# Performance work log

Measured on AMD Instinct MI355X. Metric: run time of the kernel, lower is better.

Reference implementation:

```python
import jax, jax.numpy as jnp
import numpy as np

L, D, NH, DH, K = 2, 128, 4, 32, 3  # blocks, latent_dim, heads, head_dim, kernel

def _ln(x, eps=1e-6):
    mu = x.mean(-1, keepdims=True)
    var = x.var(-1, keepdims=True)
    return (x - mu) / jnp.sqrt(var + eps)

def setup_inputs() -> dict:
    key = jax.random.key(0)
    ks = jax.random.split(key, 12)
    B, Hd, Wd = 2, 64, 96
    s = 0.02
    p = lambda k, shape: jax.random.normal(k, shape, jnp.float32) * s
    return {
        'feat_map': jax.random.normal(ks[0], (B, D, Hd, Wd), jnp.float32),
        'feat_map_up': jax.random.normal(ks[1], (B, D, 2 * Hd, 2 * Wd), jnp.float32),
        'nc_w': jnp.ones((L, D), jnp.float32), 'nc_b': jnp.zeros((L, D), jnp.float32),
        'wq': p(ks[2], (L, D, D)), 'bq': jnp.zeros((L, D), jnp.float32),
        'wkv': p(ks[3], (L, D, 2 * D)), 'bkv': jnp.zeros((L, 2 * D), jnp.float32),
        'wo': p(ks[4], (L, D, D)), 'bo': jnp.zeros((L, D), jnp.float32),
        'w1': p(ks[5], (L, D, 4 * D)), 'b1': jnp.zeros((L, 4 * D), jnp.float32),
        'w2': p(ks[6], (L, 4 * D, D)), 'b2': jnp.zeros((L, D), jnp.float32),
        'wqf': p(ks[7], (D, D)), 'bqf': jnp.zeros((D,), jnp.float32),
        'wcf': p(ks[8], (D, D)), 'bcf': jnp.zeros((D,), jnp.float32),
        'upsample_factor': 2,
    }

def reference(feat_map, feat_map_up, nc_w, nc_b, wq, bq, wkv, bkv, wo, bo,
              w1, b1, w2, b2, wqf, bqf, wcf, bcf, upsample_factor):
    B, C, Hd, Wd = feat_map.shape
    Hu, Wu = Hd * upsample_factor, Wd * upsample_factor
    N = B * Hu * Wu
    # ---- local 3x3 context via replicate-pad + shifted slices (== pad+unfold) ----
    pad = jnp.pad(feat_map, ((0, 0), (0, 0), (1, 1), (1, 1)), mode='edge')
    patches = jnp.stack([pad[:, :, i:i + Hd, j:j + Wd]
                         for i in range(K) for j in range(K)], axis=2)  # [B,C,9,Hd,Wd]
    # nearest-neighbor upsample by factor (== F.interpolate nearest)
    patches = jnp.repeat(jnp.repeat(patches, upsample_factor, axis=-2),
                         upsample_factor, axis=-1)                      # [B,C,9,Hu,Wu]
    context = patches.transpose(0, 3, 4, 2, 1).reshape(N, K * K, C)     # [(b h w),9,C]
    x = feat_map_up.transpose(0, 2, 3, 1).reshape(N, 1, C)              # [(b h w),1,C]
    scale = 1.0 / float(np.sqrt(DH))
    for l in range(L):
        # cross-attn: x = x + Attn(norm1(x), norm_ctx(context))
        ctx_n = _ln(context) * nc_w[l] + nc_b[l]
        q = _ln(x) @ wq[l] + bq[l]
        kv = ctx_n @ wkv[l] + bkv[l]
        k_, v_ = kv[..., :D], kv[..., D:]
        qh = q.reshape(N, 1, NH, DH).transpose(0, 2, 1, 3)       # [N,h,1,dh]
        kh = k_.reshape(N, K * K, NH, DH).transpose(0, 2, 1, 3)  # [N,h,9,dh]
        vh = v_.reshape(N, K * K, NH, DH).transpose(0, 2, 1, 3)
        attn = jax.nn.softmax(jnp.einsum('nhqd,nhkd->nhqk', qh, kh) * scale, axis=-1)
        o = jnp.einsum('nhqk,nhkd->nhqd', attn, vh).transpose(0, 2, 1, 3).reshape(N, 1, D)
        x = x + (o @ wo[l] + bo[l])
        # MLP: x = x + W2 gelu(W1 norm2(x))
        h = jax.nn.gelu(_ln(x) @ w1[l] + b1[l])  # tanh-approx gelu
        x = x + (h @ w2[l] + b2[l])
    # ---- final query-context attention mask ----
    xq = _ln(x) @ wqf + bqf
    ctxp = _ln(context) @ wcf + bcf
    logits = jnp.einsum('nqc,nkc->nqk', xq, ctxp) * (1.0 / float(np.sqrt(D)))
    attn_mask = jax.nn.softmax(logits, axis=-1)              # [N,1,9]
    return attn_mask.reshape(B, Hu, Wu, K * K).transpose(0, 3, 1, 2)  # [B,9,Hu,Wu]
```

## Files before the change

kernel.cpp:

```cpp
#include <hip/hip_runtime.h>

namespace {

constexpr int THREADS = 256;
constexpr int HdC = 64, WdC = 96, HuC = 128, WuC = 192;


__device__ __forceinline__ float gelu_tanh(float x) {
  float z = 0.7978845608028654f * (x + 0.044715f * x * x * x);
  float e = __expf(2.0f * z);
  float t = 1.0f - 2.0f / (e + 1.0f);
  return 0.5f * x * (1.0f + t);
}

__device__ __forceinline__ unsigned short f2bf(float f) {
  unsigned int u = __builtin_bit_cast(unsigned int, f);
  u = (u + 0x7FFFu + ((u >> 16) & 1u)) >> 16;
  return (unsigned short)u;
}

__device__ __forceinline__ float bf2f(unsigned short u) {
  unsigned int x = ((unsigned int)u) << 16;
  return __builtin_bit_cast(float, x);
}


constexpr int CTX_S = 80;
constexpr int KV_S  = 132;
constexpr int XS_S  = 132;
constexpr int XN_S  = 32;
constexpr int OB_S  = 144;

constexpr int SC_ATT = 0;
constexpr int SC_RED = 0;
constexpr int SC_MU  = 768;
constexpr int SC_RS  = 864;
constexpr int SC_NC  = 1152;
constexpr int SC_LG  = 0;

struct alignas(16) Smem {
  float ctxT[128 * CTX_S];
  float kvb[72 * KV_S];
  float xs[32 * XS_S];
  float xnT[128 * XN_S];
  float outb[32 * OB_S];
  float wbuf[32 * 128];
  float scratch[1536];
};
static_assert(sizeof(Smem) <= 160 * 1024, "LDS budget");

__device__ __forceinline__ void stage_w(const float* __restrict__ W, int wstride,
                                        int kc, float* wbuf, int tid) {
#pragma unroll
  for (int p = 0; p < 4; ++p) {
    int e = tid + p * THREADS;
    int r = e >> 5;
    int c4 = (e & 31) << 2;
    const float4 v = *reinterpret_cast<const float4*>(W + (kc * 32 + r) * wstride + c4);
    *reinterpret_cast<float4*>(wbuf + r * 128 + c4) = v;
  }
}

#define FMA_ROW(ac, s, w)                                            \
  {                                                                  \
    (ac)[0] += (s) * (w).x; (ac)[1] += (s) * (w).y;                  \
    (ac)[2] += (s) * (w).z; (ac)[3] += (s) * (w).w;                  \
  }

__device__ __forceinline__ void gemm32(const float* __restrict__ W, int wstride,
                                       const float* AT, float* wbuf, int tid,
                                       float acc[16]) {
  const int row0 = (tid >> 5) << 2;
  const int col0 = (tid & 31) << 2;
#pragma unroll
  for (int i = 0; i < 16; ++i) acc[i] = 0.f;
  for (int kc = 0; kc < 4; ++kc) {
    __syncthreads();
    stage_w(W, wstride, kc, wbuf, tid);
    __syncthreads();
#pragma unroll 4
    for (int cl = 0; cl < 32; ++cl) {
      const int c = (kc << 5) + cl;
      const float4 a = *reinterpret_cast<const float4*>(AT + c * XN_S + row0);
      const float4 w = *reinterpret_cast<const float4*>(wbuf + cl * 128 + col0);
      FMA_ROW(acc + 0, a.x, w);
      FMA_ROW(acc + 4, a.y, w);
      FMA_ROW(acc + 8, a.z, w);
      FMA_ROW(acc + 12, a.w, w);
    }
  }
}

template <bool NC>
__device__ __forceinline__ void gemm96(const float* __restrict__ W, int wstride,
                                       const float* ctxT, float* wbuf, float* kvb,
                                       const float* __restrict__ bias,
                                       const float* nc, int tid) {
  const int rt4 = (tid >> 5) << 2;
  const int col0 = (tid & 31) << 2;
  float acc[48];
#pragma unroll
  for (int i = 0; i < 48; ++i) acc[i] = 0.f;
  for (int kc = 0; kc < 4; ++kc) {
    __syncthreads();
    stage_w(W, wstride, kc, wbuf, tid);
    __syncthreads();
#pragma unroll 2
    for (int cl = 0; cl < 32; ++cl) {
      const int c = (kc << 5) + cl;
      const float4 w = *reinterpret_cast<const float4*>(wbuf + cl * 128 + col0);
      float s = 0.f, t = 0.f;
      if (NC) { s = nc[c]; t = nc[128 + c]; }
      const float* base = ctxT + c * CTX_S;
#pragma unroll
      for (int p = 0; p < 3; ++p) {
        int r0 = p * 32 + rt4;
        if (r0 > 76) r0 = 76;
        float4 a = *reinterpret_cast<const float4*>(base + r0);
        if (NC) {
          a.x = a.x * s + t; a.y = a.y * s + t;
          a.z = a.z * s + t; a.w = a.w * s + t;
        }
        float* ac = acc + p * 16;
        FMA_ROW(ac + 0, a.x, w);
        FMA_ROW(ac + 4, a.y, w);
        FMA_ROW(ac + 8, a.z, w);
        FMA_ROW(ac + 12, a.w, w);
      }
    }
  }
  const float4 bv = *reinterpret_cast<const float4*>(bias + col0);
#pragma unroll
  for (int p = 0; p < 3; ++p) {
    const int r0 = p * 32 + rt4;
    if (r0 < 72) {
#pragma unroll
      for (int i = 0; i < 4; ++i) {
        float4 o;
        o.x = acc[p * 16 + i * 4 + 0] + bv.x;
        o.y = acc[p * 16 + i * 4 + 1] + bv.y;
        o.z = acc[p * 16 + i * 4 + 2] + bv.z;
        o.w = acc[p * 16 + i * 4 + 3] + bv.w;
        *reinterpret_cast<float4*>(kvb + (r0 + i) * KV_S + col0) = o;
      }
    }
  }
}

__device__ __forceinline__ void layernorm_x(const float* xs, float* xnT,
                                            float* scratch, int tid) {
  const int px = tid & 31;
  const int cg = tid >> 5;
  float s1 = 0.f, s2 = 0.f;
#pragma unroll
  for (int i = 0; i < 16; ++i) {
    const float v = xs[px * XS_S + cg * 16 + i];
    s1 += v; s2 += v * v;
  }
  scratch[SC_RED + cg * 96 + px] = s1;
  scratch[SC_RED + cg * 96 + 48 + px] = s2;
  __syncthreads();
  if (tid < 32) {
    float a = 0.f, b = 0.f;
#pragma unroll
    for (int g = 0; g < 8; ++g) {
      a += scratch[SC_RED + g * 96 + tid];
      b += scratch[SC_RED + g * 96 + 48 + tid];
    }
    const float m = a * (1.f / 128.f);
    const float v = b * (1.f / 128.f) - m * m;
    scratch[SC_MU + tid] = m;
    scratch[SC_RS + tid] = rsqrtf(v + 1e-6f);
  }
  __syncthreads();
  const float m = scratch[SC_MU + px];
  const float r = scratch[SC_RS + px];
#pragma unroll
  for (int i = 0; i < 16; ++i) {
    const int c = cg * 16 + i;
    xnT[c * XN_S + px] = (xs[px * XS_S + c] - m) * r;
  }
}

__global__ __launch_bounds__(THREADS, 1) void fused_interp_kernel(
    const float* __restrict__ fm, const float* __restrict__ fmu,
    const float* __restrict__ nc_w, const float* __restrict__ nc_b,
    const float* __restrict__ wq, const float* __restrict__ bq,
    const float* __restrict__ wkv, const float* __restrict__ bkv,
    const float* __restrict__ wo, const float* __restrict__ bo,
    const float* __restrict__ w1, const float* __restrict__ b1,
    const float* __restrict__ w2, const float* __restrict__ b2,
    const float* __restrict__ wqf, const float* __restrict__ bqf,
    const float* __restrict__ wcf, const float* __restrict__ bcf,
    float* __restrict__ out) {
  __shared__ Smem sm;
  const int tid = threadIdx.x;
  const int bx = blockIdx.x;
  const int by = blockIdx.y;
  const int bz = blockIdx.z;
  const int lh0 = by * 2, lw0 = bx * 4;
  const int hu0 = by * 4, wu0 = bx * 8;

#pragma unroll
  for (int p = 0; p < 16; ++p) {
    const int idx = tid + p * THREADS;
    const int c = idx >> 5;
    const int px = idx & 31;
    const int hu = hu0 + (px >> 3);
    const int wu = wu0 + (px & 7);
    sm.xs[px * XS_S + c] = fmu[((bz * 128 + c) * HuC + hu) * WuC + wu];
  }

  for (int pass = 0; pass < 2; ++pass) {
    const int rl = tid >> 2;
    const int sub = tid & 3;
    const int r = pass * 64 + rl;
    const bool act = (r < 72);
    int base = 0;
    if (act) {
      const int lr = r / 9, kk = r % 9;
      const int hdp = lh0 + (lr >> 2);
      const int wdp = lw0 + (lr & 3);
      const int ki = kk / 3, kj = kk % 3;
      int hs = hdp + ki - 1; hs = hs < 0 ? 0 : (hs > HdC - 1 ? HdC - 1 : hs);
      int ws = wdp + kj - 1; ws = ws < 0 ? 0 : (ws > WdC - 1 ? WdC - 1 : ws);
      base = (bz * 128) * HdC * WdC + hs * WdC + ws;
      float s1 = 0.f, s2 = 0.f;
      for (int i = 0; i < 32; ++i) {
        const float v = fm[base + (sub * 32 + i) * (HdC * WdC)];
        s1 += v; s2 += v * v;
      }
      sm.scratch[SC_RED + sub * 64 + rl] = s1;
      sm.scratch[SC_RED + 384 + sub * 64 + rl] = s2;
    }
    __syncthreads();
    if (tid < 64 && pass * 64 + tid < 72) {
      float a = 0.f, b = 0.f;
#pragma unroll
      for (int s = 0; s < 4; ++s) {
        a += sm.scratch[SC_RED + s * 64 + tid];
        b += sm.scratch[SC_RED + 384 + s * 64 + tid];
      }
      const float m = a * (1.f / 128.f);
      const float v = b * (1.f / 128.f) - m * m;
      sm.scratch[SC_MU + pass * 64 + tid] = m;
      sm.scratch[SC_RS + pass * 64 + tid] = rsqrtf(v + 1e-6f);
    }
    __syncthreads();
    if (act) {
      const float m = sm.scratch[SC_MU + r];
      const float rr = sm.scratch[SC_RS + r];
      for (int i = 0; i < 32; ++i) {
        const int c = sub * 32 + i;
        const float v = fm[base + c * (HdC * WdC)];
        sm.ctxT[c * CTX_S + r] = (v - m) * rr;
      }
    }
    __syncthreads();
  }
  if (tid < 128) {
#pragma unroll
    for (int r = 72; r < 80; ++r) sm.ctxT[tid * CTX_S + r] = 0.f;
  }
  __syncthreads();

  const int row0 = (tid >> 5) << 2;
  const int col0 = (tid & 31) << 2;
  float acc[16];

  for (int l = 0; l < 2; ++l) {
    if (tid < 128) sm.scratch[SC_NC + tid] = nc_w[l * 128 + tid];
    else           sm.scratch[SC_NC + tid] = nc_b[l * 128 + (tid - 128)];

    layernorm_x(sm.xs, sm.xnT, sm.scratch, tid);
    gemm32(wq + l * 16384, 128, sm.xnT, sm.wbuf, tid, acc);
    {
      const float4 bv = *reinterpret_cast<const float4*>(bq + l * 128 + col0);
#pragma unroll
      for (int i = 0; i < 4; ++i) {
        float4 o;
        o.x = acc[i * 4 + 0] + bv.x; o.y = acc[i * 4 + 1] + bv.y;
        o.z = acc[i * 4 + 2] + bv.z; o.w = acc[i * 4 + 3] + bv.w;
        *reinterpret_cast<float4*>(sm.outb + (row0 + i) * OB_S + col0) = o;
      }
    }
    gemm96<true>(wkv + l * 32768, 256, sm.ctxT, sm.wbuf, sm.kvb,
                 bkv + l * 256, sm.scratch + SC_NC, tid);
    __syncthreads();
    if (tid < 128) {
      const int px = tid >> 2, h = tid & 3;
      const int lr = (((px >> 3) >> 1) << 2) | ((px & 7) >> 1);
      const float* qrow = sm.outb + px * OB_S + h * 32;
      float4 q[8];
#pragma unroll
      for (int d = 0; d < 8; ++d) q[d] = *reinterpret_cast<const float4*>(qrow + d * 4);
      float lg[9];
      float mx = -1e30f;
#pragma unroll
      for (int kk = 0; kk < 9; ++kk) {
        const float* krow = sm.kvb + (lr * 9 + kk) * KV_S + h * 32;
        float s = 0.f;
#pragma unroll
        for (int d = 0; d < 8; ++d) {
          const float4 kv = *reinterpret_cast<const float4*>(krow + d * 4);
          s += q[d].x * kv.x + q[d].y * kv.y + q[d].z * kv.z + q[d].w * kv.w;
        }
        s *= 0.17677669529663687f;
        lg[kk] = s;
        mx = fmaxf(mx, s);
      }
      float sum = 0.f;
#pragma unroll
      for (int kk = 0; kk < 9; ++kk) { lg[kk] = __expf(lg[kk] - mx); sum += lg[kk]; }
      const float inv = 1.f / sum;
#pragma unroll
      for (int kk = 0; kk < 9; ++kk)
        sm.scratch[SC_ATT + (px * 4 + h) * 9 + kk] = lg[kk] * inv;
    }
    __syncthreads();
    gemm96<true>(wkv + l * 32768 + 128, 256, sm.ctxT, sm.wbuf, sm.kvb,
                 bkv + l * 256 + 128, sm.scratch + SC_NC, tid);
    __syncthreads();
    {
      const int c = tid & 127, pg = tid >> 7;
      const int h = c >> 5;
#pragma unroll 4
      for (int i = 0; i < 16; ++i) {
        const int px = pg * 16 + i;
        const int lr = (((px >> 3) >> 1) << 2) | ((px & 7) >> 1);
        const float* aw = sm.scratch + SC_ATT + (px * 4 + h) * 9;
        float s = 0.f;
#pragma unroll
        for (int kk = 0; kk < 9; ++kk) s += aw[kk] * sm.kvb[(lr * 9 + kk) * KV_S + c];
        sm.xnT[c * XN_S + px] = s;
      }
    }
    gemm32(wo + l * 16384, 128, sm.xnT, sm.wbuf, tid, acc);
    {
      const float4 bv = *reinterpret_cast<const float4*>(bo + l * 128 + col0);
#pragma unroll
      for (int i = 0; i < 4; ++i) {
        float* xr = sm.xs + (row0 + i) * XS_S + col0;
        float4 x = *reinterpret_cast<float4*>(xr);
        x.x += acc[i * 4 + 0] + bv.x; x.y += acc[i * 4 + 1] + bv.y;
        x.z += acc[i * 4 + 2] + bv.z; x.w += acc[i * 4 + 3] + bv.w;
        *reinterpret_cast<float4*>(xr) = x;
      }
    }
    __syncthreads();
    layernorm_x(sm.xs, sm.xnT, sm.scratch, tid);
    float xd[16];
#pragma unroll
    for (int i = 0; i < 16; ++i) xd[i] = 0.f;
    for (int cc = 0; cc < 4; ++cc) {
      gemm32(w1 + l * 65536 + cc * 128, 512, sm.xnT, sm.wbuf, tid, acc);
      {
        const float4 bv = *reinterpret_cast<const float4*>(b1 + l * 512 + cc * 128 + col0);
#pragma unroll
        for (int i = 0; i < 4; ++i) {
          float4 o;
          o.x = gelu_tanh(acc[i * 4 + 0] + bv.x);
          o.y = gelu_tanh(acc[i * 4 + 1] + bv.y);
          o.z = gelu_tanh(acc[i * 4 + 2] + bv.z);
          o.w = gelu_tanh(acc[i * 4 + 3] + bv.w);
          *reinterpret_cast<float4*>(sm.outb + (row0 + i) * OB_S + col0) = o;
        }
      }
      __syncthreads();
      const float* w2c = w2 + l * 65536 + cc * 16384;
      for (int kc = 0; kc < 4; ++kc) {
        __syncthreads();
        stage_w(w2c, 128, kc, sm.wbuf, tid);
        __syncthreads();
#pragma unroll 4
        for (int cl = 0; cl < 32; ++cl) {
          const int c = (kc << 5) + cl;
          const float a0 = sm.outb[(row0 + 0) * OB_S + c];
          const float a1 = sm.outb[(row0 + 1) * OB_S + c];
          const float a2 = sm.outb[(row0 + 2) * OB_S + c];
          const float a3 = sm.outb[(row0 + 3) * OB_S + c];
          const float4 w = *reinterpret_cast<const float4*>(sm.wbuf + cl * 128 + col0);
          FMA_ROW(xd + 0, a0, w);
          FMA_ROW(xd + 4, a1, w);
          FMA_ROW(xd + 8, a2, w);
          FMA_ROW(xd + 12, a3, w);
        }
      }
    }
    {
      const float4 bv = *reinterpret_cast<const float4*>(b2 + l * 128 + col0);
#pragma unroll
      for (int i = 0; i < 4; ++i) {
        float* xr = sm.xs + (row0 + i) * XS_S + col0;
        float4 x = *reinterpret_cast<float4*>(xr);
        x.x += xd[i * 4 + 0] + bv.x; x.y += xd[i * 4 + 1] + bv.y;
        x.z += xd[i * 4 + 2] + bv.z; x.w += xd[i * 4 + 3] + bv.w;
        *reinterpret_cast<float4*>(xr) = x;
      }
    }
    __syncthreads();
  }

  layernorm_x(sm.xs, sm.xnT, sm.scratch, tid);
  gemm32(wqf, 128, sm.xnT, sm.wbuf, tid, acc);
  {
    const float4 bv = *reinterpret_cast<const float4*>(bqf + col0);
#pragma unroll
    for (int i = 0; i < 4; ++i) {
      float4 o;
      o.x = acc[i * 4 + 0] + bv.x; o.y = acc[i * 4 + 1] + bv.y;
      o.z = acc[i * 4 + 2] + bv.z; o.w = acc[i * 4 + 3] + bv.w;
      *reinterpret_cast<float4*>(sm.outb + (row0 + i) * OB_S + col0) = o;
    }
  }
  gemm96<false>(wcf, 128, sm.ctxT, sm.wbuf, sm.kvb, bcf, nullptr, tid);
  __syncthreads();
  {
    const int px = tid >> 3, sub = tid & 7;
    const int lr = (((px >> 3) >> 1) << 2) | ((px & 7) >> 1);
    const float* qrow = sm.outb + px * OB_S;
    {
      const float* crow = sm.kvb + (lr * 9 + sub) * KV_S;
      float s = 0.f;
#pragma unroll 8
      for (int c = 0; c < 128; c += 4) {
        const float4 qv = *reinterpret_cast<const float4*>(qrow + c);
        const float4 cv = *reinterpret_cast<const float4*>(crow + c);
        s += qv.x * cv.x + qv.y * cv.y + qv.z * cv.z + qv.w * cv.w;
      }
      sm.scratch[SC_LG + px * 12 + sub] = s;
    }
    if (sub == 0) {
      const float* crow = sm.kvb + (lr * 9 + 8) * KV_S;
      float s = 0.f;
#pragma unroll 8
      for (int c = 0; c < 128; c += 4) {
        const float4 qv = *reinterpret_cast<const float4*>(qrow + c);
        const float4 cv = *reinterpret_cast<const float4*>(crow + c);
        s += qv.x * cv.x + qv.y * cv.y + qv.z * cv.z + qv.w * cv.w;
      }
      sm.scratch[SC_LG + px * 12 + 8] = s;
    }
  }
  __syncthreads();
  if (tid < 32) {
    const int px = tid;
    const int hu = hu0 + (px >> 3), wu = wu0 + (px & 7);
    float lg[9], mx = -1e30f;
#pragma unroll
    for (int kk = 0; kk < 9; ++kk) {
      lg[kk] = sm.scratch[SC_LG + px * 12 + kk] * 0.08838834764831845f;
      mx = fmaxf(mx, lg[kk]);
    }
    float sum = 0.f;
#pragma unroll
    for (int kk = 0; kk < 9; ++kk) { lg[kk] = __expf(lg[kk] - mx); sum += lg[kk]; }
    const float inv = 1.f / sum;
#pragma unroll
    for (int kk = 0; kk < 9; ++kk)
      out[((bz * 9 + kk) * HuC + hu) * WuC + wu] = lg[kk] * inv;
  }
}


constexpr int PANEL = 16384;
constexpr int N_PANELS = 26;
constexpr size_t WS_NEEDED = (size_t)N_PANELS * PANEL * 2 + 2048;
constexpr int CBS = 136;
constexpr int XTS = 132;

constexpr int MSC_ATT = 0;
constexpr int MSC_LN  = 1152;
constexpr int MSC_ST  = 1408;
constexpr int MSC_N   = 1472;

typedef __attribute__((ext_vector_type(8))) short bf16x8;
typedef __attribute__((ext_vector_type(4))) float f32x4;
typedef __attribute__((ext_vector_type(8))) unsigned short u16x8;

struct alignas(16) SmemM {
  unsigned short ctxn[80 * CBS];
  unsigned short kvb[80 * CBS];
  unsigned short xn[32 * CBS];
  unsigned short hb[32 * CBS];
  unsigned short outb[32 * CBS];
  float scratch[MSC_N];
};
static_assert(sizeof(SmemM) <= 80 * 1024, "LDS budget (need 2 blocks/CU)");

__global__ void prep_weights(
    const float* __restrict__ nc_w, const float* __restrict__ nc_b,
    const float* __restrict__ wq, const float* __restrict__ wkv,
    const float* __restrict__ bkv,
    const float* __restrict__ wo, const float* __restrict__ w1,
    const float* __restrict__ w2, const float* __restrict__ wqf,
    const float* __restrict__ wcf,
    unsigned short* __restrict__ wsp, float* __restrict__ wsb) {
  const int b = blockIdx.x;
  const int t = threadIdx.x;
  if (b >= 104) {
    const int l = b - 104;
    float acc = bkv[l * 256 + t];
    for (int k = 0; k < 128; ++k)
      acc += nc_b[l * 128 + k] * wkv[l * 32768 + k * 256 + t];
    wsb[l * 256 + t] = acc;
    return;
  }
  const int pid = b >> 2, qtr = b & 3;
  const float* src = wqf; int N = 128, koff = 0, noff = 0;
  const float* sc = nullptr;
  if (pid < 24) {
    const int l = pid / 12, loc = pid % 12;
    if (loc == 0)      { src = wq + l * 16384;  N = 128; }
    else if (loc == 1) { src = wkv + l * 32768; N = 256; sc = nc_w + l * 128; }
    else if (loc == 2) { src = wkv + l * 32768; N = 256; noff = 128; sc = nc_w + l * 128; }
    else if (loc == 3) { src = wo + l * 16384;  N = 128; }
    else if (loc < 8)  { src = w1 + l * 65536;  N = 512; noff = (loc - 4) * 128; }
    else               { src = w2 + l * 65536;  N = 128; koff = (loc - 8) * 128; }
  } else if (pid == 25) { src = wcf; }
  unsigned short* dst = wsp + pid * PANEL;
#pragma unroll
  for (int p = 0; p < 2; ++p) {
    const int e = t + p * 256;
    const int n = e & 127;
    const int kg = e >> 7;
    const int k0 = qtr * 32 + kg * 8;
    unsigned short tmp[8];
#pragma unroll
    for (int i = 0; i < 8; ++i) {
      const float s = sc ? sc[k0 + i] : 1.f;
      tmp[i] = f2bf(src[(k0 + i + koff) * N + noff + n] * s);
    }
    *reinterpret_cast<u16x8*>(dst + n * 128 + k0) = *reinterpret_cast<u16x8*>(tmp);
  }
}

__device__ __forceinline__ void load_b8(const unsigned short* __restrict__ W,
                                        bf16x8 b[2][4], int nl, int q8, int w2t) {
#pragma unroll
  for (int t = 0; t < 2; ++t)
#pragma unroll
    for (int ks = 0; ks < 4; ++ks)
      b[t][ks] = *reinterpret_cast<const bf16x8*>(
          W + ((w2t + t) * 16 + nl) * 128 + ks * 32 + q8);
}

__device__ __forceinline__ void mfma32v(const unsigned short* A, const bf16x8 b[2][4],
                                        f32x4 acc[4], int nl, int q8, bool init) {
  if (init) {
#pragma unroll
    for (int i = 0; i < 4; ++i) acc[i] = (f32x4){0.f, 0.f, 0.f, 0.f};
  }
#pragma unroll
  for (int ks = 0; ks < 4; ++ks) {
    const bf16x8 a0 = *reinterpret_cast<const bf16x8*>(A + nl * CBS + ks * 32 + q8);
    const bf16x8 a1 = *reinterpret_cast<const bf16x8*>(A + (16 + nl) * CBS + ks * 32 + q8);
    acc[0] = __builtin_amdgcn_mfma_f32_16x16x32_bf16(a0, b[0][ks], acc[0], 0, 0, 0);
    acc[1] = __builtin_amdgcn_mfma_f32_16x16x32_bf16(a0, b[1][ks], acc[1], 0, 0, 0);
    acc[2] = __builtin_amdgcn_mfma_f32_16x16x32_bf16(a1, b[0][ks], acc[2], 0, 0, 0);
    acc[3] = __builtin_amdgcn_mfma_f32_16x16x32_bf16(a1, b[1][ks], acc[3], 0, 0, 0);
  }
}

__device__ __forceinline__ void mfma72v(const unsigned short* Ctx, const bf16x8 b[2][4],
                                        f32x4 acc[10], int nl, int q8) {
#pragma unroll
  for (int i = 0; i < 10; ++i) acc[i] = (f32x4){0.f, 0.f, 0.f, 0.f};
#pragma unroll
  for (int ks = 0; ks < 4; ++ks) {
    const bf16x8 b0 = b[0][ks], b1 = b[1][ks];
#pragma unroll
    for (int rt = 0; rt < 5; ++rt) {
      const bf16x8 a = *reinterpret_cast<const bf16x8*>(
          Ctx + (rt * 16 + nl) * CBS + ks * 32 + q8);
      acc[rt * 2 + 0] = __builtin_amdgcn_mfma_f32_16x16x32_bf16(a, b0, acc[rt * 2 + 0], 0, 0, 0);
      acc[rt * 2 + 1] = __builtin_amdgcn_mfma_f32_16x16x32_bf16(a, b1, acc[rt * 2 + 1], 0, 0, 0);
    }
  }
}

__device__ __forceinline__ void ln_x(const float (&xr)[2][2][4], unsigned short* xn,
                                     float* scratch, int wave, int nl, int qm) {
#pragma unroll
  for (int rt = 0; rt < 2; ++rt)
#pragma unroll
    for (int r = 0; r < 4; ++r) {
      float s1 = xr[rt][0][r] + xr[rt][1][r];
      float s2 = xr[rt][0][r] * xr[rt][0][r] + xr[rt][1][r] * xr[rt][1][r];
#pragma unroll
      for (int m = 1; m < 16; m <<= 1) {
        s1 += __shfl_xor(s1, m, 64);
        s2 += __shfl_xor(s2, m, 64);
      }
      if (nl == 0) {
        const int px = rt * 16 + qm + r;
        scratch[MSC_LN + px * 4 + wave] = s1;
        scratch[MSC_LN + 128 + px * 4 + wave] = s2;
      }
    }
  __syncthreads();
#pragma unroll
  for (int rt = 0; rt < 2; ++rt)
#pragma unroll
    for (int r = 0; r < 4; ++r) {
      const int px = rt * 16 + qm + r;
      float a = 0.f, b = 0.f;
#pragma unroll
      for (int w = 0; w < 4; ++w) {
        a += scratch[MSC_LN + px * 4 + w];
        b += scratch[MSC_LN + 128 + px * 4 + w];
      }
      const float m = a * (1.f / 128.f);
      const float v = b * (1.f / 128.f) - m * m;
      const float rs = rsqrtf(v + 1e-6f);
#pragma unroll
      for (int t = 0; t < 2; ++t)
        xn[px * CBS + (wave * 2 + t) * 16 + nl] = f2bf((xr[rt][t][r] - m) * rs);
    }
  __syncthreads();
}

__global__ __launch_bounds__(THREADS, 2) void fused_interp_mfma(
    const float* __restrict__ fm, const float* __restrict__ fmu,
    const float* __restrict__ bq, const float* __restrict__ bo,
    const float* __restrict__ b1, const float* __restrict__ b2,
    const float* __restrict__ bqf, const float* __restrict__ bcf,
    const unsigned short* __restrict__ wsp, const float* __restrict__ wsb,
    float* __restrict__ out) {
  __shared__ SmemM sm;
  const int tid = threadIdx.x;
  const int bx = blockIdx.x, by = blockIdx.y, bz = blockIdx.z;
  const int lh0 = by * 2, lw0 = bx * 4;
  const int hu0 = by * 4, wu0 = bx * 8;

  const int lane = tid & 63;
  const int wave = tid >> 6;
  const int nl = lane & 15;
  const int q8 = (lane >> 4) * 8;
  const int qm = (lane >> 4) * 4;
  const int w2t = wave * 2;

  {
    float* xtmp = reinterpret_cast<float*>(sm.ctxn);
#pragma unroll
    for (int p = 0; p < 8; ++p) {
      const int e = tid + p * THREADS;
      const int pe = e & 15;
      const int c = e >> 4;
      const int hu = hu0 + (pe >> 2);
      const int wu = wu0 + (pe & 3) * 2;
      const float2 v = *reinterpret_cast<const float2*>(
          &fmu[((bz * 128 + c) * HuC + hu) * WuC + wu]);
      const int px = (pe >> 2) * 8 + (pe & 3) * 2;
      xtmp[px * XTS + c] = v.x;
      xtmp[(px + 1) * XTS + c] = v.y;
    }
  }
  __syncthreads();
  float xr[2][2][4];
  {
    const float* xtmp = reinterpret_cast<const float*>(sm.ctxn);
#pragma unroll
    for (int rt = 0; rt < 2; ++rt)
#pragma unroll
      for (int t = 0; t < 2; ++t)
#pragma unroll
        for (int r = 0; r < 4; ++r)
          xr[rt][t][r] = xtmp[(rt * 16 + qm + r) * XTS + (w2t + t) * 16 + nl];
  }
  __syncthreads();

  bf16x8 Bq[2][4], Bk[2][4], Bv[2][4], Bo[2][4], B1[2][4], B2[2][4];
  load_b8(wsp + 0 * PANEL, Bq, nl, q8, w2t);
  load_b8(wsp + 1 * PANEL, Bk, nl, q8, w2t);

  {
    float* patch = reinterpret_cast<float*>(sm.kvb);
#pragma unroll
    for (int p = 0; p < 12; ++p) {
      const int e = tid + p * THREADS;
      const int c = e / 24;
      const int rem = e - c * 24;
      const int hs_i = rem / 6;
      const int ws_i = rem - hs_i * 6;
      int hd = lh0 - 1 + hs_i; hd = hd < 0 ? 0 : (hd > HdC - 1 ? HdC - 1 : hd);
      int wd = lw0 - 1 + ws_i; wd = wd < 0 ? 0 : (wd > WdC - 1 ? WdC - 1 : wd);
      patch[(hs_i * 6 + ws_i) * XTS + c] = fm[((bz * 128 + c) * HdC + hd) * WdC + wd];
    }
  }
  __syncthreads();
  {
    const float* patch = reinterpret_cast<const float*>(sm.kvb);
    if (tid < 192) {
      const int pp = tid >> 3, part = tid & 7;
      float s1 = 0.f, s2 = 0.f;
#pragma unroll
      for (int i = 0; i < 16; ++i) {
        const float v = patch[pp * XTS + part * 16 + i];
        s1 += v; s2 += v * v;
      }
      sm.scratch[MSC_ATT + tid * 2 + 0] = s1;
      sm.scratch[MSC_ATT + tid * 2 + 1] = s2;
    }
    __syncthreads();
    if (tid < 24) {
      float a = 0.f, b = 0.f;
#pragma unroll
      for (int g = 0; g < 8; ++g) {
        a += sm.scratch[MSC_ATT + (tid * 8 + g) * 2 + 0];
        b += sm.scratch[MSC_ATT + (tid * 8 + g) * 2 + 1];
      }
      const float m = a * (1.f / 128.f);
      const float v = b * (1.f / 128.f) - m * m;
      sm.scratch[MSC_ST + tid * 2 + 0] = m;
      sm.scratch[MSC_ST + tid * 2 + 1] = rsqrtf(v + 1e-6f);
    }
    __syncthreads();
#pragma unroll
    for (int p = 0; p < 5; ++p) {
      const int e = tid + p * THREADS;
      if (e < 1152) {
        const int r = e >> 4, cg = e & 15;
        const int lr = r / 9;
        const int kk = r - lr * 9;
        const int ki = kk / 3, kj = kk - ki * 3;
        const int pp = ((lr >> 2) + ki) * 6 + (lr & 3) + kj;
        const float m = sm.scratch[MSC_ST + pp * 2 + 0];
        const float rs = sm.scratch[MSC_ST + pp * 2 + 1];
        unsigned short tmp[8];
#pragma unroll
        for (int j = 0; j < 8; ++j)
          tmp[j] = f2bf((patch[pp * XTS + cg * 8 + j] - m) * rs);
        *reinterpret_cast<u16x8*>(sm.ctxn + r * CBS + cg * 8) = *reinterpret_cast<u16x8*>(tmp);
      }
    }
  }
  __syncthreads();

  f32x4 acc4[4];
  f32x4 acc10[10];

  for (int l = 0; l < 2; ++l) {
    const unsigned short* P = wsp + (l * 12) * PANEL;

    float kb[2], vb[2], bqr[2], bor[2], b2r[2], b1r[4][2];
#pragma unroll
    for (int t = 0; t < 2; ++t) {
      const int n = (w2t + t) * 16 + nl;
      kb[t] = wsb[l * 256 + n];
      vb[t] = wsb[l * 256 + 128 + n];
      bqr[t] = bq[l * 128 + n];
      bor[t] = bo[l * 128 + n];
      b2r[t] = b2[l * 128 + n];
#pragma unroll
      for (int cc = 0; cc < 4; ++cc) b1r[cc][t] = b1[l * 512 + cc * 128 + n];
    }

    ln_x(xr, sm.xn, sm.scratch, wave, nl, qm);

    mfma32v(sm.xn, Bq, acc4, nl, q8, true);
#pragma unroll
    for (int rt = 0; rt < 2; ++rt)
#pragma unroll
      for (int t = 0; t < 2; ++t) {
        const int n = (w2t + t) * 16 + nl;
#pragma unroll
        for (int r = 0; r < 4; ++r)
          sm.outb[(rt * 16 + qm + r) * CBS + n] = f2bf(acc4[rt * 2 + t][r] + bqr[t]);
      }
    mfma72v(sm.ctxn, Bk, acc10, nl, q8);
    load_b8(P + 2 * PANEL, Bv, nl, q8, w2t);
#pragma unroll
    for (int t = 0; t < 2; ++t) {
      const int n = (w2t + t) * 16 + nl;
#pragma unroll
      for (int rt = 0; rt < 5; ++rt)
#pragma unroll
        for (int r = 0; r < 4; ++r) {
          const int row = rt * 16 + qm + r;
          if (row < 72) sm.kvb[row * CBS + n] = f2bf(acc10[rt * 2 + t][r] + kb[t]);
        }
    }
    __syncthreads();

    mfma72v(sm.ctxn, Bv, acc10, nl, q8);
    load_b8(P + 3 * PANEL, Bo, nl, q8, w2t);

    {
      const int u = tid >> 1, sub = tid & 1;
      const int px = u >> 2, h = u & 3;
      const int lr = (((px >> 3) >> 1) << 2) | ((px & 7) >> 1);
      const unsigned short* qrow = sm.outb + px * CBS + h * 32;
      float qf[32];
#pragma unroll
      for (int c8 = 0; c8 < 4; ++c8) {
        const u16x8 qa = *reinterpret_cast<const u16x8*>(qrow + c8 * 8);
#pragma unroll
        for (int j = 0; j < 8; ++j) qf[c8 * 8 + j] = bf2f(qa[j]);
      }
      const int base = sub ? 5 : 0;
      const int cnt = sub ? 4 : 5;
      float mine[5];
#pragma unroll
      for (int i = 0; i < 5; ++i) {
        float s = 0.f;
        if (i < cnt) {
          const unsigned short* krow = sm.kvb + (lr * 9 + base + i) * CBS + h * 32;
#pragma unroll
          for (int c8 = 0; c8 < 4; ++c8) {
            const u16x8 ka = *reinterpret_cast<const u16x8*>(krow + c8 * 8);
#pragma unroll
            for (int j = 0; j < 8; ++j) s += qf[c8 * 8 + j] * bf2f(ka[j]);
          }
          s *= 0.17677669529663687f;
        }
        mine[i] = s;
      }
      float other[5];
#pragma unroll
      for (int i = 0; i < 5; ++i) other[i] = __shfl_xor(mine[i], 1, 64);
      float lg[9];
#pragma unroll
      for (int j = 0; j < 5; ++j) lg[j] = sub ? other[j] : mine[j];
#pragma unroll
      for (int j = 0; j < 4; ++j) lg[5 + j] = sub ? mine[j] : other[j];
      float mx = -1e30f;
#pragma unroll
      for (int kk = 0; kk < 9; ++kk) mx = fmaxf(mx, lg[kk]);
      float sum = 0.f;
#pragma unroll
      for (int kk = 0; kk < 9; ++kk) { lg[kk] = __expf(lg[kk] - mx); sum += lg[kk]; }
      const float inv = 1.f / sum;
#pragma unroll
      for (int j = 0; j < 5; ++j)
        if (j < cnt) sm.scratch[MSC_ATT + (px * 4 + h) * 9 + base + j] = lg[base + j] * inv;
    }
    __syncthreads();

#pragma unroll
    for (int t = 0; t < 2; ++t) {
      const int n = (w2t + t) * 16 + nl;
#pragma unroll
      for (int rt = 0; rt < 5; ++rt)
#pragma unroll
        for (int r = 0; r < 4; ++r) {
          const int row = rt * 16 + qm + r;
          if (row < 72) sm.kvb[row * CBS + n] = f2bf(acc10[rt * 2 + t][r] + vb[t]);
        }
    }
    __syncthreads();

    {
      const int px = tid >> 3, cg = tid & 7, c0 = cg * 16;
      const int lr = (((px >> 3) >> 1) << 2) | ((px & 7) >> 1);
      const float* aw = sm.scratch + MSC_ATT + (px * 4 + (cg >> 1)) * 9;
      float o[16];
#pragma unroll
      for (int j = 0; j < 16; ++j) o[j] = 0.f;
#pragma unroll
      for (int kk = 0; kk < 9; ++kk) {
        const float a = aw[kk];
        const unsigned short* vrow = sm.kvb + (lr * 9 + kk) * CBS + c0;
        const u16x8 v0 = *reinterpret_cast<const u16x8*>(vrow);
        const u16x8 v1 = *reinterpret_cast<const u16x8*>(vrow + 8);
#pragma unroll
        for (int j = 0; j < 8; ++j) {
          o[j] += a * bf2f(v0[j]);
          o[8 + j] += a * bf2f(v1[j]);
        }
      }
      unsigned short tmp[16];
#pragma unroll
      for (int j = 0; j < 16; ++j) tmp[j] = f2bf(o[j]);
      *reinterpret_cast<u16x8*>(sm.xn + px * CBS + c0) = *reinterpret_cast<u16x8*>(tmp);
      *reinterpret_cast<u16x8*>(sm.xn + px * CBS + c0 + 8) = *reinterpret_cast<u16x8*>(tmp + 8);
    }
    load_b8(P + 4 * PANEL, B1, nl, q8, w2t);
    __syncthreads();

    mfma32v(sm.xn, Bo, acc4, nl, q8, true);
#pragma unroll
    for (int rt = 0; rt < 2; ++rt)
#pragma unroll
      for (int t = 0; t < 2; ++t)
#pragma unroll
        for (int r = 0; r < 4; ++r)
          xr[rt][t][r] += acc4[rt * 2 + t][r] + bor[t];

    ln_x(xr, sm.xn, sm.scratch, wave, nl, qm);
    f32x4 xd[4];
    for (int cc = 0; cc < 4; ++cc) {
      mfma32v(sm.xn, B1, acc4, nl, q8, true);
      load_b8(P + (8 + cc) * PANEL, B2, nl, q8, w2t);
#pragma unroll
      for (int rt = 0; rt < 2; ++rt)
#pragma unroll
        for (int t = 0; t < 2; ++t) {
          const int n = (w2t + t) * 16 + nl;
#pragma unroll
          for (int r = 0; r < 4; ++r)
            sm.hb[(rt * 16 + qm + r) * CBS + n] =
                f2bf(gelu_tanh(acc4[rt * 2 + t][r] + b1r[cc][t]));
        }
      __syncthreads();
      if (cc < 3) load_b8(P + (5 + cc) * PANEL, B1, nl, q8, w2t);
      mfma32v(sm.hb, B2, xd, nl, q8, cc == 0);
      if (cc < 3) __syncthreads();
    }
#pragma unroll
    for (int rt = 0; rt < 2; ++rt)
#pragma unroll
      for (int t = 0; t < 2; ++t)
#pragma unroll
        for (int r = 0; r < 4; ++r)
          xr[rt][t][r] += xd[rt * 2 + t][r] + b2r[t];

    if (l == 0) {
      load_b8(wsp + 12 * PANEL, Bq, nl, q8, w2t);
      load_b8(wsp + 13 * PANEL, Bk, nl, q8, w2t);
    } else {
      load_b8(wsp + 24 * PANEL, Bq, nl, q8, w2t);
      load_b8(wsp + 25 * PANEL, Bk, nl, q8, w2t);
    }
  }

  float bqfr[2], bcfr[2];
#pragma unroll
  for (int t = 0; t < 2; ++t) {
    const int n = (w2t + t) * 16 + nl;
    bqfr[t] = bqf[n];
    bcfr[t] = bcf[n];
  }
  ln_x(xr, sm.xn, sm.scratch, wave, nl, qm);
  mfma32v(sm.xn, Bq, acc4, nl, q8, true);
#pragma unroll
  for (int rt = 0; rt < 2; ++rt)
#pragma unroll
    for (int t = 0; t < 2; ++t) {
      const int n = (w2t + t) * 16 + nl;
#pragma unroll
      for (int r = 0; r < 4; ++r)
        sm.outb[(rt * 16 + qm + r) * CBS + n] = f2bf(acc4[rt * 2 + t][r] + bqfr[t]);
    }
  mfma72v(sm.ctxn, Bk, acc10, nl, q8);
#pragma unroll
  for (int t = 0; t < 2; ++t) {
    const int n = (w2t + t) * 16 + nl;
#pragma unroll
    for (int rt = 0; rt < 5; ++rt)
#pragma unroll
      for (int r = 0; r < 4; ++r) {
        const int row = rt * 16 + qm + r;
        if (row < 72) sm.kvb[row * CBS + n] = f2bf(acc10[rt * 2 + t][r] + bcfr[t]);
      }
  }
  __syncthreads();
  {
    const int px = tid >> 3, sub = tid & 7;
    const int lr = (((px >> 3) >> 1) << 2) | ((px & 7) >> 1);
    const unsigned short* qrow = sm.outb + px * CBS;
#pragma unroll
    for (int which = 0; which < 2; ++which) {
      if (which == 1 && sub != 0) break;
      const int kk = (which == 0) ? sub : 8;
      const unsigned short* crow = sm.kvb + (lr * 9 + kk) * CBS;
      float s = 0.f;
#pragma unroll
      for (int c8 = 0; c8 < 16; ++c8) {
        const u16x8 qa = *reinterpret_cast<const u16x8*>(qrow + c8 * 8);
        const u16x8 ca = *reinterpret_cast<const u16x8*>(crow + c8 * 8);
#pragma unroll
        for (int j = 0; j < 8; ++j) s += bf2f(qa[j]) * bf2f(ca[j]);
      }
      sm.scratch[MSC_ATT + px * 12 + kk] = s;
    }
  }
  __syncthreads();
  if (tid < 32) {
    const int px = tid;
    const int hu = hu0 + (px >> 3), wu = wu0 + (px & 7);
    float lg[9], mx = -1e30f;
#pragma unroll
    for (int kk = 0; kk < 9; ++kk) {
      lg[kk] = sm.scratch[MSC_ATT + px * 12 + kk] * 0.08838834764831845f;
      mx = fmaxf(mx, lg[kk]);
    }
    float sum = 0.f;
#pragma unroll
    for (int kk = 0; kk < 9; ++kk) { lg[kk] = __expf(lg[kk] - mx); sum += lg[kk]; }
    const float inv = 1.f / sum;
#pragma unroll
    for (int kk = 0; kk < 9; ++kk)
      out[((bz * 9 + kk) * HuC + hu) * WuC + wu] = lg[kk] * inv;
  }
}

}

extern "C" void kernel_launch(void* const* d_in, const int* in_sizes, int n_in,
                              void* d_out, int out_size, void* d_ws, size_t ws_size,
                              hipStream_t stream) {
  const float* fm   = (const float*)d_in[0];
  const float* fmu  = (const float*)d_in[1];
  const float* nc_w = (const float*)d_in[2];
  const float* nc_b = (const float*)d_in[3];
  const float* wq   = (const float*)d_in[4];
  const float* bq   = (const float*)d_in[5];
  const float* wkv  = (const float*)d_in[6];
  const float* bkv  = (const float*)d_in[7];
  const float* wo   = (const float*)d_in[8];
  const float* bo   = (const float*)d_in[9];
  const float* w1   = (const float*)d_in[10];
  const float* b1   = (const float*)d_in[11];
  const float* w2   = (const float*)d_in[12];
  const float* b2   = (const float*)d_in[13];
  const float* wqf  = (const float*)d_in[14];
  const float* bqf  = (const float*)d_in[15];
  const float* wcf  = (const float*)d_in[16];
  const float* bcf  = (const float*)d_in[17];
  float* out = (float*)d_out;

  dim3 grid(24, 32, 2);
  if (ws_size >= WS_NEEDED) {
    unsigned short* wsp = (unsigned short*)d_ws;
    float* wsb = (float*)((char*)d_ws + (size_t)N_PANELS * PANEL * 2);
    prep_weights<<<dim3(106), dim3(256), 0, stream>>>(
        nc_w, nc_b, wq, wkv, bkv, wo, w1, w2, wqf, wcf, wsp, wsb);
    fused_interp_mfma<<<grid, dim3(THREADS), 0, stream>>>(
        fm, fmu, bq, bo, b1, b2, bqf, bcf, wsp, wsb, out);
  } else {
    fused_interp_kernel<<<grid, dim3(THREADS), 0, stream>>>(
        fm, fmu, nc_w, nc_b, wq, bq, wkv, bkv, wo, bo, w1, b1, w2, b2,
        wqf, bqf, wcf, bcf, out);
  }
}
```

Measured before the change: 363.3 us.

## Reduce weight-fragment registers to two rotating buffers and reorder V projection

Replaces six live bf16 weight fragment arrays with two rotating buffers (Ba/Bb), loading each panel just before use. The V projection MFMA is moved after the QK softmax phase so K and V results never hold acc10 at the same time. The Q·K dot loop is also restructured to stream q chunks rather than holding a 32-float q array. The aim is to cut VGPR pressure, possibly raising occupancy or avoiding spills. The cost is less lookahead on weight loads, since prefetch distance shrinks and load latency may be exposed.

Result: faster. 305.5 us (-15.9%).

```diff
diff --git a/kernel.cpp b/kernel.cpp
--- a/kernel.cpp
+++ b/kernel.cpp
@@ -670,10 +670,6 @@
   }
   __syncthreads();
 
-  bf16x8 Bq[2][4], Bk[2][4], Bv[2][4], Bo[2][4], B1[2][4], B2[2][4];
-  load_b8(wsp + 0 * PANEL, Bq, nl, q8, w2t);
-  load_b8(wsp + 1 * PANEL, Bk, nl, q8, w2t);
-
   {
     float* patch = reinterpret_cast<float*>(sm.kvb);
 #pragma unroll
@@ -739,6 +735,7 @@
 
   f32x4 acc4[4];
   f32x4 acc10[10];
+  bf16x8 Ba[2][4], Bb[2][4];
 
   for (int l = 0; l < 2; ++l) {
     const unsigned short* P = wsp + (l * 12) * PANEL;
@@ -756,9 +753,11 @@
       for (int cc = 0; cc < 4; ++cc) b1r[cc][t] = b1[l * 512 + cc * 128 + n];
     }
 
+    load_b8(P + 0 * PANEL, Ba, nl, q8, w2t);
+    load_b8(P + 1 * PANEL, Bb, nl, q8, w2t);
     ln_x(xr, sm.xn, sm.scratch, wave, nl, qm);
 
-    mfma32v(sm.xn, Bq, acc4, nl, q8, true);
+    mfma32v(sm.xn, Ba, acc4, nl, q8, true);
 #pragma unroll
     for (int rt = 0; rt < 2; ++rt)
 #pragma unroll
@@ -768,8 +767,8 @@
         for (int r = 0; r < 4; ++r)
           sm.outb[(rt * 16 + qm + r) * CBS + n] = f2bf(acc4[rt * 2 + t][r] + bqr[t]);
       }
-    mfma72v(sm.ctxn, Bk, acc10, nl, q8);
-    load_b8(P + 2 * PANEL, Bv, nl, q8, w2t);
+    mfma72v(sm.ctxn, Bb, acc10, nl, q8);
+    load_b8(P + 2 * PANEL, Ba, nl, q8, w2t);
 #pragma unroll
     for (int t = 0; t < 2; ++t) {
       const int n = (w2t + t) * 16 + nl;
@@ -782,40 +781,37 @@
         }
     }
     __syncthreads();
-
-    mfma72v(sm.ctxn, Bv, acc10, nl, q8);
-    load_b8(P + 3 * PANEL, Bo, nl, q8, w2t);
 
     {
       const int u = tid >> 1, sub = tid & 1;
       const int px = u >> 2, h = u & 3;
       const int lr = (((px >> 3) >> 1) << 2) | ((px & 7) >> 1);
       const unsigned short* qrow = sm.outb + px * CBS + h * 32;
-      float qf[32];
-#pragma unroll
-      for (int c8 = 0; c8 < 4; ++c8) {
-        const u16x8 qa = *reinterpret_cast<const u16x8*>(qrow + c8 * 8);
-#pragma unroll
-        for (int j = 0; j < 8; ++j) qf[c8 * 8 + j] = bf2f(qa[j]);
-      }
       const int base = sub ? 5 : 0;
       const int cnt = sub ? 4 : 5;
       float mine[5];
 #pragma unroll
-      for (int i = 0; i < 5; ++i) {
-        float s = 0.f;
-        if (i < cnt) {
-          const unsigned short* krow = sm.kvb + (lr * 9 + base + i) * CBS + h * 32;
-#pragma unroll
-          for (int c8 = 0; c8 < 4; ++c8) {
-            const u16x8 ka = *reinterpret_cast<const u16x8*>(krow + c8 * 8);
-#pragma unroll
-            for (int j = 0; j < 8; ++j) s += qf[c8 * 8 + j] * bf2f(ka[j]);
+      for (int i = 0; i < 5; ++i) mine[i] = 0.f;
+#pragma unroll
+      for (int c8 = 0; c8 < 4; ++c8) {
+        const u16x8 qa = *reinterpret_cast<const u16x8*>(qrow + c8 * 8);
+        float qaf[8];
+#pragma unroll
+        for (int j = 0; j < 8; ++j) qaf[j] = bf2f(qa[j]);
+#pragma unroll
+        for (int i = 0; i < 5; ++i) {
+          if (i < cnt) {
+            const u16x8 ka = *reinterpret_cast<const u16x8*>(
+                sm.kvb + (lr * 9 + base + i) * CBS + h * 32 + c8 * 8);
+            float s = 0.f;
+#pragma unroll
+            for (int j = 0; j < 8; ++j) s += qaf[j] * bf2f(ka[j]);
+            mine[i] += s;
           }
-          s *= 0.17677669529663687f;
         }
-        mine[i] = s;
-      }
+      }
+#pragma unroll
+      for (int i = 0; i < 5; ++i) mine[i] *= 0.17677669529663687f;
       float other[5];
 #pragma unroll
       for (int i = 0; i < 5; ++i) other[i] = __shfl_xor(mine[i], 1, 64);
@@ -837,6 +833,8 @@
     }
     __syncthreads();
 
+    mfma72v(sm.ctxn, Ba, acc10, nl, q8);
+    load_b8(P + 3 * PANEL, Bb, nl, q8, w2t);
 #pragma unroll
     for (int t = 0; t < 2; ++t) {
       const int n = (w2t + t) * 16 + nl;
@@ -875,10 +873,9 @@
       *reinterpret_cast<u16x8*>(sm.xn + px * CBS + c0) = *reinterpret_cast<u16x8*>(tmp);
       *reinterpret_cast<u16x8*>(sm.xn + px * CBS + c0 + 8) = *reinterpret_cast<u16x8*>(tmp + 8);
     }
-    load_b8(P + 4 * PANEL, B1, nl, q8, w2t);
-    __syncthreads();
-
-    mfma32v(sm.xn, Bo, acc4, nl, q8, true);
+    __syncthreads();
+
+    mfma32v(sm.xn, Bb, acc4, nl, q8, true);
 #pragma unroll
     for (int rt = 0; rt < 2; ++rt)
 #pragma unroll
@@ -887,11 +884,12 @@
         for (int r = 0; r < 4; ++r)
           xr[rt][t][r] += acc4[rt * 2 + t][r] + bor[t];
 
+    load_b8(P + 4 * PANEL, Ba, nl, q8, w2t);
     ln_x(xr, sm.xn, sm.scratch, wave, nl, qm);
     f32x4 xd[4];
     for (int cc = 0; cc < 4; ++cc) {
-      mfma32v(sm.xn, B1, acc4, nl, q8, true);
-      load_b8(P + (8 + cc) * PANEL, B2, nl, q8, w2t);
+      mfma32v(sm.xn, Ba, acc4, nl, q8, true);
+      load_b8(P + (8 + cc) * PANEL, Bb, nl, q8, w2t);
 #pragma unroll
       for (int rt = 0; rt < 2; ++rt)
 #pragma unroll
@@ -903,8 +901,8 @@
                 f2bf(gelu_tanh(acc4[rt * 2 + t][r] + b1r[cc][t]));
         }
       __syncthreads();
-      if (cc < 3) load_b8(P + (5 + cc) * PANEL, B1, nl, q8, w2t);
-      mfma32v(sm.hb, B2, xd, nl, q8, cc == 0);
+      if (cc < 3) load_b8(P + (5 + cc) * PANEL, Ba, nl, q8, w2t);
+      mfma32v(sm.hb, Bb, xd, nl, q8, cc == 0);
       if (cc < 3) __syncthreads();
     }
 #pragma unroll
@@ -914,14 +912,6 @@
 #pragma unroll
         for (int r = 0; r < 4; ++r)
           xr[rt][t][r] += xd[rt * 2 + t][r] + b2r[t];
-
-    if (l == 0) {
-      load_b8(wsp + 12 * PANEL, Bq, nl, q8, w2t);
-      load_b8(wsp + 13 * PANEL, Bk, nl, q8, w2t);
-    } else {
-      load_b8(wsp + 24 * PANEL, Bq, nl, q8, w2t);
-      load_b8(wsp + 25 * PANEL, Bk, nl, q8, w2t);
-    }
   }
 
   float bqfr[2], bcfr[2];
@@ -931,8 +921,10 @@
     bqfr[t] = bqf[n];
     bcfr[t] = bcf[n];
   }
+  load_b8(wsp + 24 * PANEL, Ba, nl, q8, w2t);
+  load_b8(wsp + 25 * PANEL, Bb, nl, q8, w2t);
   ln_x(xr, sm.xn, sm.scratch, wave, nl, qm);
-  mfma32v(sm.xn, Bq, acc4, nl, q8, true);
+  mfma32v(sm.xn, Ba, acc4, nl, q8, true);
 #pragma unroll
   for (int rt = 0; rt < 2; ++rt)
 #pragma unroll
@@ -942,7 +934,7 @@
       for (int r = 0; r < 4; ++r)
         sm.outb[(rt * 16 + qm + r) * CBS + n] = f2bf(acc4[rt * 2 + t][r] + bqfr[t]);
     }
-  mfma72v(sm.ctxn, Bk, acc10, nl, q8);
+  mfma72v(sm.ctxn, Bb, acc10, nl, q8);
 #pragma unroll
   for (int t = 0; t < 2; ++t) {
     const int n = (w2t + t) * 16 + nl;
```
